# Kernel tuning notes

Measured on AMD Instinct MI355X. Metric: run time of the kernel, lower is better.

## Reference

```python
import jax, jax.numpy as jnp
import numpy as np

DIM = 512
HID = 1536          # int(2*(4*512)/3) rounded up to multiple of 256
N_EXPERTS = 8
TOP_K = 2
SHARED_HID = HID * 2  # n_shared_experts scales hidden dim of the single shared MLP
B, S = 4, 2048


def _swiglu(x, w1, w3, w2):
    return (jax.nn.silu(x @ w1.T) * (x @ w3.T)) @ w2.T


def setup_inputs() -> dict:
    key = jax.random.key(0)
    ks = jax.random.split(key, 8)
    sc_d = 1.0 / np.sqrt(DIM)
    sc_h = 1.0 / np.sqrt(HID)
    sc_sh = 1.0 / np.sqrt(SHARED_HID)
    return {
        "x": jax.random.normal(ks[0], (B, S, DIM), jnp.float32),
        "gate_w": jax.random.normal(ks[1], (N_EXPERTS, DIM), jnp.float32) * sc_d,
        "w1": jax.random.normal(ks[2], (N_EXPERTS, HID, DIM), jnp.float32) * sc_d,
        "w3": jax.random.normal(ks[3], (N_EXPERTS, HID, DIM), jnp.float32) * sc_d,
        "w2": jax.random.normal(ks[4], (N_EXPERTS, DIM, HID), jnp.float32) * sc_h,
        "sw1": jax.random.normal(ks[5], (SHARED_HID, DIM), jnp.float32) * sc_d,
        "sw3": jax.random.normal(ks[6], (SHARED_HID, DIM), jnp.float32) * sc_d,
        "sw2": jax.random.normal(ks[7], (DIM, SHARED_HID), jnp.float32) * sc_sh,
    }


def reference(x, gate_w, w1, w3, w2, sw1, sw3, sw2):
    b, s, d = x.shape
    t = b * s
    xf = x.reshape(t, d)

    # --- gate (greedy top-k over softmax scores, fp32) ---
    logits = xf.astype(jnp.float32) @ gate_w.astype(jnp.float32).T  # [T, E]
    scores = jax.nn.softmax(logits, axis=-1)
    topk_w, topk_i = jax.lax.top_k(scores, TOP_K)                    # [T, K]

    # per-token combine weight for each expert: sum of topk weights routed to it
    e = gate_w.shape[0]
    comb = jnp.zeros((t, e), jnp.float32).at[jnp.arange(t)[:, None], topk_i].add(topk_w)

    # --- routed experts: weighted sum of SwiGLU outputs ---
    y = jnp.zeros((t, d), x.dtype)
    for i in range(e):  # fixed small number of structurally distinct experts
        ye = _swiglu(xf, w1[i], w3[i], w2[i]).astype(x.dtype)
        y = y + comb[:, i:i + 1].astype(x.dtype) * ye
    y = y.reshape(b, s, d)

    # --- shared expert added to all tokens ---
    shared = _swiglu(xf, sw1, sw3, sw2).reshape(b, s, d).astype(x.dtype)
    return y + shared
```

## Files before the change

kernel.cpp:

```cpp
#include <hip/hip_runtime.h>

#define T_TOK 8192
#define DIMSZ 512
#define HIDSZ 1536
#define SHIDSZ 3072
#define NE 8

typedef __attribute__((ext_vector_type(4))) float f32x4;
typedef __attribute__((ext_vector_type(8))) short s16x8;

__device__ __forceinline__ unsigned short f2bf(float f) {
  unsigned int u = __float_as_uint(f);
  u += 0x7fff + ((u >> 16) & 1);
  return (unsigned short)(u >> 16);
}

__device__ __forceinline__ void async16(void* lds, const void* g) {
  __builtin_amdgcn_global_load_lds((const __attribute__((address_space(1))) void*)g,
                                   (__attribute__((address_space(3))) void*)lds,
                                   16, 0, 0);
}

__global__ void cvt_bf16(const float* __restrict__ s, unsigned short* __restrict__ d, int n4) {
  int i = blockIdx.x * blockDim.x + threadIdx.x;
  if (i < n4) {
    float4 v = ((const float4*)s)[i];
    ushort4 o;
    o.x = f2bf(v.x); o.y = f2bf(v.y); o.z = f2bf(v.z); o.w = f2bf(v.w);
    ((ushort4*)d)[i] = o;
  }
}

#define GATE_BLOCKS 256
#define GATE_TPB (T_TOK / GATE_BLOCKS)
#define GATE_TPW (GATE_TPB / 4)

__global__ __launch_bounds__(256) void gate_kernel(
    const float* __restrict__ x, const float* __restrict__ gw,
    float* __restrict__ tw, int* __restrict__ ti, int* __restrict__ cnt) {
  __shared__ int lcnt[NE];
  const int tid = threadIdx.x;
  if (tid < NE) lcnt[tid] = 0;
  __syncthreads();
  const int w = tid >> 6, l = tid & 63;

  float gv[NE][8];
  const float* gbase = gw + l * 8;
#pragma unroll
  for (int e = 0; e < NE; ++e)
#pragma unroll
    for (int j = 0; j < 8; ++j) gv[e][j] = gbase[e * DIMSZ + j];

  const int tok0 = blockIdx.x * GATE_TPB + w * GATE_TPW;
  for (int it = 0; it < GATE_TPW; ++it) {
    const int t = tok0 + it;
    const float* xr = x + (size_t)t * DIMSZ + l * 8;
    float xv[8];
#pragma unroll
    for (int j = 0; j < 8; ++j) xv[j] = xr[j];
    float p[NE];
#pragma unroll
    for (int e = 0; e < NE; ++e) {
      float s = 0.f;
#pragma unroll
      for (int j = 0; j < 8; ++j) s = fmaf(xv[j], gv[e][j], s);
      p[e] = s;
    }
#pragma unroll
    for (int e = 0; e < NE; ++e) {
      float v = p[e];
#pragma unroll
      for (int off = 32; off > 0; off >>= 1) v += __shfl_xor(v, off);
      p[e] = v;
    }
    float m = p[0];
#pragma unroll
    for (int e = 1; e < NE; ++e) m = fmaxf(m, p[e]);
    float ex[NE], s = 0.f;
#pragma unroll
    for (int e = 0; e < NE; ++e) { ex[e] = __expf(p[e] - m); s += ex[e]; }
    float inv = 1.f / s;
    int e0 = 0; float v0 = p[0];
#pragma unroll
    for (int e = 1; e < NE; ++e) if (p[e] > v0) { v0 = p[e]; e0 = e; }
    int e1 = -1; float v1 = -3.4e38f;
#pragma unroll
    for (int e = 0; e < NE; ++e) if (e != e0 && p[e] > v1) { v1 = p[e]; e1 = e; }
    if (l == 0) {
      ti[2 * t] = e0;     tw[2 * t] = ex[e0] * inv;
      ti[2 * t + 1] = e1; tw[2 * t + 1] = ex[e1] * inv;
      atomicAdd(&lcnt[e0], 1);
      atomicAdd(&lcnt[e1], 1);
    }
  }
  __syncthreads();
  if (tid < NE) atomicAdd(&cnt[tid], lcnt[tid]);
}

__global__ void scan_kernel(const int* __restrict__ cnt, int* __restrict__ base,
                            int* __restrict__ cursor) {
  if (threadIdx.x == 0 && blockIdx.x == 0) {
    int r = 0;
    for (int e = 0; e < NE; ++e) { base[e] = r; cursor[e] = r; r += cnt[e]; }
  }
}

__global__ __launch_bounds__(256) void scatter_kernel(
    const int* __restrict__ ti, int* __restrict__ cursor,
    int* __restrict__ tok, int* __restrict__ dst) {
  __shared__ int lcnt[NE], gbase[NE];
  const int tid = threadIdx.x;
  if (tid < NE) lcnt[tid] = 0;
  __syncthreads();
  const int t = blockIdx.x * 256 + tid;
  const int e0 = ti[2 * t], e1 = ti[2 * t + 1];
  const int p0 = atomicAdd(&lcnt[e0], 1);
  const int p1 = atomicAdd(&lcnt[e1], 1);
  __syncthreads();
  if (tid < NE) gbase[tid] = atomicAdd(&cursor[tid], lcnt[tid]);
  __syncthreads();
  const int i0 = gbase[e0] + p0, i1 = gbase[e1] + p1;
  tok[i0] = t; dst[i0] = 2 * t;
  tok[i1] = t; dst[i1] = 2 * t + 1;
}

__global__ void gather_kernel(const unsigned short* __restrict__ xb,
                              const int* __restrict__ tok,
                              unsigned short* __restrict__ xg) {
  int i = blockIdx.x * blockDim.x + threadIdx.x;
  int entry = i >> 6, l = i & 63;
  int t = tok[entry];
  ((uint4*)xg)[entry * 64 + l] = ((const uint4*)xb)[t * 64 + l];
}


template <bool ROUTED>
__global__ __launch_bounds__(256, 3) void gemm1_kernel(
    const unsigned short* __restrict__ A0, const unsigned short* __restrict__ W1,
    const unsigned short* __restrict__ W3, unsigned short* __restrict__ G,
    const int* __restrict__ cnt, const int* __restrict__ base,
    int K, int N, int mtPerE) {
  int e, mt, cntE, rowbase;
  if constexpr (ROUTED) {
    e = blockIdx.x / mtPerE; mt = blockIdx.x % mtPerE;
    cntE = cnt[e];
    if (mt * 128 >= cntE) return;
    rowbase = base[e];
  } else {
    e = 0; mt = blockIdx.x; cntE = T_TOK; rowbase = 0;
  }
  const int m0 = mt * 128;
  const int n0 = blockIdx.y * 64;
  const unsigned short* A = A0 + (size_t)rowbase * K;
  const unsigned short* B1 = W1 + (size_t)e * N * K + (size_t)n0 * K;
  const unsigned short* B3 = W3 + (size_t)e * N * K + (size_t)n0 * K;

  __shared__ __align__(16) unsigned short As[128 * 64];
  __shared__ __align__(16) unsigned short B1s[64 * 64];
  __shared__ __align__(16) unsigned short B3s[64 * 64];

  const int tid = threadIdx.x;
  const int w = tid >> 6, lane = tid & 63;
  const int wr = w >> 1, wc = w & 1;
  const int lhi = lane >> 4, llo = lane & 15;

  const unsigned short* aSrc[4];
  unsigned short* aDst[4];
#pragma unroll
  for (int i = 0; i < 4; ++i) {
    int L = i * 256 + tid, row = L >> 3, c = L & 7, sc = c ^ (row & 7);
    int ar = ROUTED ? min(m0 + row, cntE - 1) : (m0 + row);
    aSrc[i] = A + (size_t)ar * K + sc * 8;
    aDst[i] = &As[(size_t)(i * 256 + (tid & ~63)) * 8];
  }
  const unsigned short *b1Src[2], *b3Src[2];
  unsigned short *b1Dst[2], *b3Dst[2];
#pragma unroll
  for (int i = 0; i < 2; ++i) {
    int L = i * 256 + tid, row = L >> 3, c = L & 7, sc = c ^ (row & 7);
    b1Src[i] = B1 + (size_t)row * K + sc * 8;
    b3Src[i] = B3 + (size_t)row * K + sc * 8;
    b1Dst[i] = &B1s[(size_t)(i * 256 + (tid & ~63)) * 8];
    b3Dst[i] = &B3s[(size_t)(i * 256 + (tid & ~63)) * 8];
  }

  int aOff[4][2], bOff[2][2];
#pragma unroll
  for (int m = 0; m < 4; ++m) {
    int r = wr * 64 + m * 16 + llo;
#pragma unroll
    for (int s = 0; s < 2; ++s)
      aOff[m][s] = r * 64 + (((lhi + 4 * s) ^ (r & 7)) * 8);
  }
#pragma unroll
  for (int n = 0; n < 2; ++n) {
    int r = wc * 32 + n * 16 + llo;
#pragma unroll
    for (int s = 0; s < 2; ++s)
      bOff[n][s] = r * 64 + (((lhi + 4 * s) ^ (r & 7)) * 8);
  }

  f32x4 acc1[4][2], acc3[4][2];
#pragma unroll
  for (int m = 0; m < 4; ++m)
#pragma unroll
    for (int n = 0; n < 2; ++n) {
      acc1[m][n] = f32x4{0.f, 0.f, 0.f, 0.f};
      acc3[m][n] = f32x4{0.f, 0.f, 0.f, 0.f};
    }

  for (int k0 = 0; k0 < K; k0 += 64) {
#pragma unroll
    for (int i = 0; i < 4; ++i) async16(aDst[i], aSrc[i] + k0);
#pragma unroll
    for (int i = 0; i < 2; ++i) {
      async16(b1Dst[i], b1Src[i] + k0);
      async16(b3Dst[i], b3Src[i] + k0);
    }
    __syncthreads();
#pragma unroll
    for (int s = 0; s < 2; ++s) {
      s16x8 a[4], b1f[2], b3f[2];
#pragma unroll
      for (int m = 0; m < 4; ++m) a[m] = *(const s16x8*)&As[aOff[m][s]];
#pragma unroll
      for (int n = 0; n < 2; ++n) {
        b1f[n] = *(const s16x8*)&B1s[bOff[n][s]];
        b3f[n] = *(const s16x8*)&B3s[bOff[n][s]];
      }
#pragma unroll
      for (int m = 0; m < 4; ++m)
#pragma unroll
        for (int n = 0; n < 2; ++n) {
          acc1[m][n] = __builtin_amdgcn_mfma_f32_16x16x32_bf16(a[m], b1f[n], acc1[m][n], 0, 0, 0);
          acc3[m][n] = __builtin_amdgcn_mfma_f32_16x16x32_bf16(a[m], b3f[n], acc3[m][n], 0, 0, 0);
        }
    }
    __syncthreads();
  }

  unsigned short* Grow = G + (size_t)rowbase * N;
#pragma unroll
  for (int m = 0; m < 4; ++m)
#pragma unroll
    for (int n = 0; n < 2; ++n)
#pragma unroll
      for (int q = 0; q < 4; ++q) {
        int r = wr * 64 + m * 16 + lhi * 4 + q;
        if (!ROUTED || (m0 + r) < cntE) {
          float h1 = acc1[m][n][q], h3 = acc3[m][n][q];
          float val = (h1 / (1.f + __expf(-h1))) * h3;
          Grow[(size_t)(m0 + r) * N + n0 + wc * 32 + n * 16 + llo] = f2bf(val);
        }
      }
}

template <bool ROUTED>
__global__ __launch_bounds__(256, 3) void gemm2_kernel(
    const unsigned short* __restrict__ A0, const unsigned short* __restrict__ W2,
    float* __restrict__ Out, const int* __restrict__ cnt, const int* __restrict__ base,
    const int* __restrict__ dst, int K, int mtPerE) {
  int e, mt, cntE, rowbase;
  if constexpr (ROUTED) {
    e = blockIdx.x / mtPerE; mt = blockIdx.x % mtPerE;
    cntE = cnt[e];
    if (mt * 128 >= cntE) return;
    rowbase = base[e];
  } else {
    e = 0; mt = blockIdx.x; cntE = T_TOK; rowbase = 0;
  }
  const int m0 = mt * 128;
  const int n0 = blockIdx.y * 128;
  const unsigned short* A = A0 + (size_t)rowbase * K;
  const unsigned short* B = W2 + (size_t)e * DIMSZ * K + (size_t)n0 * K;

  __shared__ __align__(16) unsigned short As[128 * 64];
  __shared__ __align__(16) unsigned short Bs[128 * 64];

  const int tid = threadIdx.x;
  const int w = tid >> 6, lane = tid & 63;
  const int wr = w >> 1, wc = w & 1;
  const int lhi = lane >> 4, llo = lane & 15;

  const unsigned short *aSrc[4], *bSrc[4];
  unsigned short *aDst[4], *bDst[4];
#pragma unroll
  for (int i = 0; i < 4; ++i) {
    int L = i * 256 + tid, row = L >> 3, c = L & 7, sc = c ^ (row & 7);
    int ar = ROUTED ? min(m0 + row, cntE - 1) : (m0 + row);
    aSrc[i] = A + (size_t)ar * K + sc * 8;
    bSrc[i] = B + (size_t)row * K + sc * 8;
    aDst[i] = &As[(size_t)(i * 256 + (tid & ~63)) * 8];
    bDst[i] = &Bs[(size_t)(i * 256 + (tid & ~63)) * 8];
  }

  int aOff[4][2], bOff[4][2];
#pragma unroll
  for (int m = 0; m < 4; ++m) {
    int ra = wr * 64 + m * 16 + llo;
    int rb = wc * 64 + m * 16 + llo;
#pragma unroll
    for (int s = 0; s < 2; ++s) {
      aOff[m][s] = ra * 64 + (((lhi + 4 * s) ^ (ra & 7)) * 8);
      bOff[m][s] = rb * 64 + (((lhi + 4 * s) ^ (rb & 7)) * 8);
    }
  }

  f32x4 acc[4][4];
#pragma unroll
  for (int i = 0; i < 4; ++i)
#pragma unroll
    for (int j = 0; j < 4; ++j) acc[i][j] = f32x4{0.f, 0.f, 0.f, 0.f};

  for (int k0 = 0; k0 < K; k0 += 64) {
#pragma unroll
    for (int i = 0; i < 4; ++i) {
      async16(aDst[i], aSrc[i] + k0);
      async16(bDst[i], bSrc[i] + k0);
    }
    __syncthreads();
#pragma unroll
    for (int s = 0; s < 2; ++s) {
      s16x8 a[4], b[4];
#pragma unroll
      for (int m = 0; m < 4; ++m) {
        a[m] = *(const s16x8*)&As[aOff[m][s]];
        b[m] = *(const s16x8*)&Bs[bOff[m][s]];
      }
#pragma unroll
      for (int i = 0; i < 4; ++i)
#pragma unroll
        for (int j = 0; j < 4; ++j)
          acc[i][j] = __builtin_amdgcn_mfma_f32_16x16x32_bf16(a[i], b[j], acc[i][j], 0, 0, 0);
    }
    __syncthreads();
  }

#pragma unroll
  for (int i = 0; i < 4; ++i)
#pragma unroll
    for (int j = 0; j < 4; ++j)
#pragma unroll
      for (int q = 0; q < 4; ++q) {
        int r = wr * 64 + i * 16 + lhi * 4 + q;
        if (!ROUTED || (m0 + r) < cntE) {
          int orow;
          if constexpr (ROUTED) orow = dst[rowbase + m0 + r];
          else                  orow = m0 + r;
          Out[(size_t)orow * DIMSZ + n0 + wc * 64 + j * 16 + llo] = acc[i][j][q];
        }
      }
}

__global__ void combine_kernel(const float* __restrict__ shbuf, const float* __restrict__ pair,
                               const float* __restrict__ tw, float* __restrict__ out) {
  int i = blockIdx.x * blockDim.x + threadIdx.x;
  int t = i >> 7, c = i & 127;
  float w0 = tw[2 * t], w1 = tw[2 * t + 1];
  float4 a = ((const float4*)shbuf)[i];
  float4 p0 = ((const float4*)pair)[(size_t)(2 * t) * 128 + c];
  float4 p1 = ((const float4*)pair)[(size_t)(2 * t + 1) * 128 + c];
  float4 o;
  o.x = a.x + w0 * p0.x + w1 * p1.x;
  o.y = a.y + w0 * p0.y + w1 * p1.y;
  o.z = a.z + w0 * p0.z + w1 * p1.z;
  o.w = a.w + w0 * p0.w + w1 * p1.w;
  ((float4*)out)[i] = o;
}

extern "C" void kernel_launch(void* const* d_in, const int* in_sizes, int n_in,
                              void* d_out, int out_size, void* d_ws, size_t ws_size,
                              hipStream_t stream) {
  const float* x   = (const float*)d_in[0];
  const float* gw  = (const float*)d_in[1];
  const float* w1  = (const float*)d_in[2];
  const float* w3  = (const float*)d_in[3];
  const float* w2  = (const float*)d_in[4];
  const float* sw1 = (const float*)d_in[5];
  const float* sw3 = (const float*)d_in[6];
  const float* sw2 = (const float*)d_in[7];
  float* out = (float*)d_out;

  char* p = (char*)d_ws;
  auto alloc = [&](size_t bytes) {
    char* r = p;
    p += (bytes + 255) & ~(size_t)255;
    return r;
  };
  unsigned short* xb   = (unsigned short*)alloc((size_t)T_TOK * DIMSZ * 2);
  unsigned short* xg   = (unsigned short*)alloc((size_t)2 * T_TOK * DIMSZ * 2);
  unsigned short* w1b  = (unsigned short*)alloc((size_t)NE * HIDSZ * DIMSZ * 2);
  unsigned short* w3b  = (unsigned short*)alloc((size_t)NE * HIDSZ * DIMSZ * 2);
  unsigned short* w2b  = (unsigned short*)alloc((size_t)NE * DIMSZ * HIDSZ * 2);
  unsigned short* sw1b = (unsigned short*)alloc((size_t)SHIDSZ * DIMSZ * 2);
  unsigned short* sw3b = (unsigned short*)alloc((size_t)SHIDSZ * DIMSZ * 2);
  unsigned short* sw2b = (unsigned short*)alloc((size_t)DIMSZ * SHIDSZ * 2);
  unsigned short* g    = (unsigned short*)alloc((size_t)T_TOK * SHIDSZ * 2);
  float* pairout = (float*)alloc((size_t)2 * T_TOK * DIMSZ * 4);
  float* shbuf   = (float*)alloc((size_t)T_TOK * DIMSZ * 4);
  float* tw = (float*)alloc((size_t)2 * T_TOK * 4);
  int* ti   = (int*)alloc((size_t)2 * T_TOK * 4);
  int* tok  = (int*)alloc((size_t)2 * T_TOK * 4);
  int* dst  = (int*)alloc((size_t)2 * T_TOK * 4);
  int* meta = (int*)alloc(256);
  int* cnt = meta, *cursor = meta + 8, *base = meta + 16;

  auto cvt = [&](const float* s, unsigned short* d, size_t n) {
    int n4 = (int)(n / 4);
    cvt_bf16<<<(n4 + 255) / 256, 256, 0, stream>>>(s, d, n4);
  };
  cvt(x, xb, (size_t)T_TOK * DIMSZ);
  cvt(w1, w1b, (size_t)NE * HIDSZ * DIMSZ);
  cvt(w3, w3b, (size_t)NE * HIDSZ * DIMSZ);
  cvt(w2, w2b, (size_t)NE * DIMSZ * HIDSZ);
  cvt(sw1, sw1b, (size_t)SHIDSZ * DIMSZ);
  cvt(sw3, sw3b, (size_t)SHIDSZ * DIMSZ);
  cvt(sw2, sw2b, (size_t)DIMSZ * SHIDSZ);

  hipMemsetAsync(meta, 0, 64, stream);
  gate_kernel<<<GATE_BLOCKS, 256, 0, stream>>>(x, gw, tw, ti, cnt);
  scan_kernel<<<1, 64, 0, stream>>>(cnt, base, cursor);
  scatter_kernel<<<T_TOK / 256, 256, 0, stream>>>(ti, cursor, tok, dst);
  gather_kernel<<<(2 * T_TOK * 64) / 256, 256, 0, stream>>>(xb, tok, xg);

  gemm1_kernel<false><<<dim3(T_TOK / 128, SHIDSZ / 64), 256, 0, stream>>>(
      xb, sw1b, sw3b, g, nullptr, nullptr, DIMSZ, SHIDSZ, T_TOK / 128);
  gemm2_kernel<false><<<dim3(T_TOK / 128, DIMSZ / 128), 256, 0, stream>>>(
      g, sw2b, shbuf, nullptr, nullptr, nullptr, SHIDSZ, T_TOK / 128);

  gemm1_kernel<true><<<dim3(NE * (T_TOK / 128), HIDSZ / 64), 256, 0, stream>>>(
      xg, w1b, w3b, g, cnt, base, DIMSZ, HIDSZ, T_TOK / 128);
  gemm2_kernel<true><<<dim3(NE * (T_TOK / 128), DIMSZ / 128), 256, 0, stream>>>(
      g, w2b, pairout, cnt, base, dst, HIDSZ, T_TOK / 128);

  combine_kernel<<<(T_TOK * 128) / 256, 256, 0, stream>>>(shbuf, pairout, tw, out);
}
```

Measured before the change: 448.7 us.

## Double-buffer LDS in both GEMMs and halve gemm2 M-tile

Both GEMM kernels now use two LDS buffers. The next K-tile is prefetched with async global-to-LDS loads while the current tile is computed, and partial vmcnt waits plus raw barriers replace the full __syncthreads pairs, so memory latency overlaps with MFMA work. gemm2 also drops from a 128-row to a 64-row M tile, which doubles its grid for better CU fill and cuts padding waste on the routed experts. The cost is doubled LDS use, which lowers gemm1's occupancy hint from 3 to 2 blocks, and less B-tile reuse in gemm2.

```diff
diff --git a/kernel.cpp b/kernel.cpp
--- a/kernel.cpp
+++ b/kernel.cpp
@@ -8,6 +8,8 @@
 
 typedef __attribute__((ext_vector_type(4))) float f32x4;
 typedef __attribute__((ext_vector_type(8))) short s16x8;
+
+#define SBAR() __builtin_amdgcn_s_barrier()
 
 __device__ __forceinline__ unsigned short f2bf(float f) {
   unsigned int u = __float_as_uint(f);
@@ -135,7 +137,7 @@
 
 
 template <bool ROUTED>
-__global__ __launch_bounds__(256, 3) void gemm1_kernel(
+__global__ __launch_bounds__(256, 2) void gemm1_kernel(
     const unsigned short* __restrict__ A0, const unsigned short* __restrict__ W1,
     const unsigned short* __restrict__ W3, unsigned short* __restrict__ G,
     const int* __restrict__ cnt, const int* __restrict__ base,
@@ -155,9 +157,9 @@
   const unsigned short* B1 = W1 + (size_t)e * N * K + (size_t)n0 * K;
   const unsigned short* B3 = W3 + (size_t)e * N * K + (size_t)n0 * K;
 
-  __shared__ __align__(16) unsigned short As[128 * 64];
-  __shared__ __align__(16) unsigned short B1s[64 * 64];
-  __shared__ __align__(16) unsigned short B3s[64 * 64];
+  __shared__ __align__(16) unsigned short As[2 * 128 * 64];
+  __shared__ __align__(16) unsigned short B1s[2 * 64 * 64];
+  __shared__ __align__(16) unsigned short B3s[2 * 64 * 64];
 
   const int tid = threadIdx.x;
   const int w = tid >> 6, lane = tid & 63;
@@ -165,23 +167,22 @@
   const int lhi = lane >> 4, llo = lane & 15;
 
   const unsigned short* aSrc[4];
-  unsigned short* aDst[4];
+  int aDst[4];
 #pragma unroll
   for (int i = 0; i < 4; ++i) {
     int L = i * 256 + tid, row = L >> 3, c = L & 7, sc = c ^ (row & 7);
     int ar = ROUTED ? min(m0 + row, cntE - 1) : (m0 + row);
     aSrc[i] = A + (size_t)ar * K + sc * 8;
-    aDst[i] = &As[(size_t)(i * 256 + (tid & ~63)) * 8];
+    aDst[i] = (i * 256 + (tid & ~63)) * 8;
   }
   const unsigned short *b1Src[2], *b3Src[2];
-  unsigned short *b1Dst[2], *b3Dst[2];
+  int bDst[2];
 #pragma unroll
   for (int i = 0; i < 2; ++i) {
     int L = i * 256 + tid, row = L >> 3, c = L & 7, sc = c ^ (row & 7);
     b1Src[i] = B1 + (size_t)row * K + sc * 8;
     b3Src[i] = B3 + (size_t)row * K + sc * 8;
-    b1Dst[i] = &B1s[(size_t)(i * 256 + (tid & ~63)) * 8];
-    b3Dst[i] = &B3s[(size_t)(i * 256 + (tid & ~63)) * 8];
+    bDst[i] = (i * 256 + (tid & ~63)) * 8;
   }
 
   int aOff[4][2], bOff[2][2];
@@ -209,24 +210,43 @@
       acc3[m][n] = f32x4{0.f, 0.f, 0.f, 0.f};
     }
 
-  for (int k0 = 0; k0 < K; k0 += 64) {
-#pragma unroll
-    for (int i = 0; i < 4; ++i) async16(aDst[i], aSrc[i] + k0);
-#pragma unroll
-    for (int i = 0; i < 2; ++i) {
-      async16(b1Dst[i], b1Src[i] + k0);
-      async16(b3Dst[i], b3Src[i] + k0);
-    }
-    __syncthreads();
+  const int nt = K >> 6;
+  int cur = 0;
+#pragma unroll
+  for (int i = 0; i < 4; ++i) async16(&As[aDst[i]], aSrc[i]);
+#pragma unroll
+  for (int i = 0; i < 2; ++i) {
+    async16(&B1s[bDst[i]], b1Src[i]);
+    async16(&B3s[bDst[i]], b3Src[i]);
+  }
+
+  for (int t = 0; t < nt; ++t) {
+    const bool more = (t + 1) < nt;
+    if (more) {
+      const int k1 = (t + 1) << 6;
+      const int nxtA = (cur ^ 1) * 8192, nxtB = (cur ^ 1) * 4096;
+#pragma unroll
+      for (int i = 0; i < 4; ++i) async16(&As[nxtA + aDst[i]], aSrc[i] + k1);
+#pragma unroll
+      for (int i = 0; i < 2; ++i) {
+        async16(&B1s[nxtB + bDst[i]], b1Src[i] + k1);
+        async16(&B3s[nxtB + bDst[i]], b3Src[i] + k1);
+      }
+      asm volatile("s_waitcnt vmcnt(8)" ::: "memory");
+    } else {
+      asm volatile("s_waitcnt vmcnt(0)" ::: "memory");
+    }
+    SBAR();
+    const int cA = cur * 8192, cB = cur * 4096;
 #pragma unroll
     for (int s = 0; s < 2; ++s) {
       s16x8 a[4], b1f[2], b3f[2];
 #pragma unroll
-      for (int m = 0; m < 4; ++m) a[m] = *(const s16x8*)&As[aOff[m][s]];
+      for (int m = 0; m < 4; ++m) a[m] = *(const s16x8*)&As[cA + aOff[m][s]];
 #pragma unroll
       for (int n = 0; n < 2; ++n) {
-        b1f[n] = *(const s16x8*)&B1s[bOff[n][s]];
-        b3f[n] = *(const s16x8*)&B3s[bOff[n][s]];
+        b1f[n] = *(const s16x8*)&B1s[cB + bOff[n][s]];
+        b3f[n] = *(const s16x8*)&B3s[cB + bOff[n][s]];
       }
 #pragma unroll
       for (int m = 0; m < 4; ++m)
@@ -236,7 +256,7 @@
           acc3[m][n] = __builtin_amdgcn_mfma_f32_16x16x32_bf16(a[m], b3f[n], acc3[m][n], 0, 0, 0);
         }
     }
-    __syncthreads();
+    if (more) { SBAR(); cur ^= 1; }
   }
 
   unsigned short* Grow = G + (size_t)rowbase * N;
@@ -264,85 +284,109 @@
   if constexpr (ROUTED) {
     e = blockIdx.x / mtPerE; mt = blockIdx.x % mtPerE;
     cntE = cnt[e];
-    if (mt * 128 >= cntE) return;
+    if (mt * 64 >= cntE) return;
     rowbase = base[e];
   } else {
     e = 0; mt = blockIdx.x; cntE = T_TOK; rowbase = 0;
   }
-  const int m0 = mt * 128;
+  const int m0 = mt * 64;
   const int n0 = blockIdx.y * 128;
   const unsigned short* A = A0 + (size_t)rowbase * K;
   const unsigned short* B = W2 + (size_t)e * DIMSZ * K + (size_t)n0 * K;
 
-  __shared__ __align__(16) unsigned short As[128 * 64];
-  __shared__ __align__(16) unsigned short Bs[128 * 64];
+  __shared__ __align__(16) unsigned short As[2 * 64 * 64];
+  __shared__ __align__(16) unsigned short Bs[2 * 128 * 64];
 
   const int tid = threadIdx.x;
   const int w = tid >> 6, lane = tid & 63;
   const int wr = w >> 1, wc = w & 1;
   const int lhi = lane >> 4, llo = lane & 15;
 
-  const unsigned short *aSrc[4], *bSrc[4];
-  unsigned short *aDst[4], *bDst[4];
-#pragma unroll
-  for (int i = 0; i < 4; ++i) {
+  const unsigned short* aSrc[2];
+  int aDst[2];
+#pragma unroll
+  for (int i = 0; i < 2; ++i) {
     int L = i * 256 + tid, row = L >> 3, c = L & 7, sc = c ^ (row & 7);
     int ar = ROUTED ? min(m0 + row, cntE - 1) : (m0 + row);
     aSrc[i] = A + (size_t)ar * K + sc * 8;
+    aDst[i] = (i * 256 + (tid & ~63)) * 8;
+  }
+  const unsigned short* bSrc[4];
+  int bDst[4];
+#pragma unroll
+  for (int i = 0; i < 4; ++i) {
+    int L = i * 256 + tid, row = L >> 3, c = L & 7, sc = c ^ (row & 7);
     bSrc[i] = B + (size_t)row * K + sc * 8;
-    aDst[i] = &As[(size_t)(i * 256 + (tid & ~63)) * 8];
-    bDst[i] = &Bs[(size_t)(i * 256 + (tid & ~63)) * 8];
-  }
-
-  int aOff[4][2], bOff[4][2];
-#pragma unroll
-  for (int m = 0; m < 4; ++m) {
-    int ra = wr * 64 + m * 16 + llo;
-    int rb = wc * 64 + m * 16 + llo;
+    bDst[i] = (i * 256 + (tid & ~63)) * 8;
+  }
+
+  int aOff[2][2], bOff[4][2];
+#pragma unroll
+  for (int m = 0; m < 2; ++m) {
+    int r = wr * 32 + m * 16 + llo;
+#pragma unroll
+    for (int s = 0; s < 2; ++s)
+      aOff[m][s] = r * 64 + (((lhi + 4 * s) ^ (r & 7)) * 8);
+  }
+#pragma unroll
+  for (int n = 0; n < 4; ++n) {
+    int r = wc * 64 + n * 16 + llo;
+#pragma unroll
+    for (int s = 0; s < 2; ++s)
+      bOff[n][s] = r * 64 + (((lhi + 4 * s) ^ (r & 7)) * 8);
+  }
+
+  f32x4 acc[2][4];
+#pragma unroll
+  for (int i = 0; i < 2; ++i)
+#pragma unroll
+    for (int j = 0; j < 4; ++j) acc[i][j] = f32x4{0.f, 0.f, 0.f, 0.f};
+
+  const int nt = K >> 6;
+  int cur = 0;
+#pragma unroll
+  for (int i = 0; i < 2; ++i) async16(&As[aDst[i]], aSrc[i]);
+#pragma unroll
+  for (int i = 0; i < 4; ++i) async16(&Bs[bDst[i]], bSrc[i]);
+
+  for (int t = 0; t < nt; ++t) {
+    const bool more = (t + 1) < nt;
+    if (more) {
+      const int k1 = (t + 1) << 6;
+      const int nxtA = (cur ^ 1) * 4096, nxtB = (cur ^ 1) * 8192;
+#pragma unroll
+      for (int i = 0; i < 2; ++i) async16(&As[nxtA + aDst[i]], aSrc[i] + k1);
+#pragma unroll
+      for (int i = 0; i < 4; ++i) async16(&Bs[nxtB + bDst[i]], bSrc[i] + k1);
+      asm volatile("s_waitcnt vmcnt(6)" ::: "memory");
+    } else {
+      asm volatile("s_waitcnt vmcnt(0)" ::: "memory");
+    }
+    SBAR();
+    const int cA = cur * 4096, cB = cur * 8192;
 #pragma unroll
     for (int s = 0; s < 2; ++s) {
-      aOff[m][s] = ra * 64 + (((lhi + 4 * s) ^ (ra & 7)) * 8);
-      bOff[m][s] = rb * 64 + (((lhi + 4 * s) ^ (rb & 7)) * 8);
-    }
-  }
-
-  f32x4 acc[4][4];
-#pragma unroll
-  for (int i = 0; i < 4; ++i)
-#pragma unroll
-    for (int j = 0; j < 4; ++j) acc[i][j] = f32x4{0.f, 0.f, 0.f, 0.f};
-
-  for (int k0 = 0; k0 < K; k0 += 64) {
-#pragma unroll
-    for (int i = 0; i < 4; ++i) {
-      async16(aDst[i], aSrc[i] + k0);
-      async16(bDst[i], bSrc[i] + k0);
-    }
-    __syncthreads();
-#pragma unroll
-    for (int s = 0; s < 2; ++s) {
-      s16x8 a[4], b[4];
-#pragma unroll
-      for (int m = 0; m < 4; ++m) {
-        a[m] = *(const s16x8*)&As[aOff[m][s]];
-        b[m] = *(const s16x8*)&Bs[bOff[m][s]];
-      }
-#pragma unroll
-      for (int i = 0; i < 4; ++i)
+      s16x8 a[2], b[4];
+#pragma unroll
+      for (int m = 0; m < 2; ++m) a[m] = *(const s16x8*)&As[cA + aOff[m][s]];
+#pragma unroll
+      for (int n = 0; n < 4; ++n) b[n] = *(const s16x8*)&Bs[cB + bOff[n][s]];
+#pragma unroll
+      for (int i = 0; i < 2; ++i)
 #pragma unroll
         for (int j = 0; j < 4; ++j)
           acc[i][j] = __builtin_amdgcn_mfma_f32_16x16x32_bf16(a[i], b[j], acc[i][j], 0, 0, 0);
     }
-    __syncthreads();
-  }
-
-#pragma unroll
-  for (int i = 0; i < 4; ++i)
+    if (more) { SBAR(); cur ^= 1; }
+  }
+
+#pragma unroll
+  for (int i = 0; i < 2; ++i)
 #pragma unroll
     for (int j = 0; j < 4; ++j)
 #pragma unroll
       for (int q = 0; q < 4; ++q) {
-        int r = wr * 64 + i * 16 + lhi * 4 + q;
+        int r = wr * 32 + i * 16 + lhi * 4 + q;
         if (!ROUTED || (m0 + r) < cntE) {
           int orow;
           if constexpr (ROUTED) orow = dst[rowbase + m0 + r];
@@ -425,13 +469,13 @@
 
   gemm1_kernel<false><<<dim3(T_TOK / 128, SHIDSZ / 64), 256, 0, stream>>>(
       xb, sw1b, sw3b, g, nullptr, nullptr, DIMSZ, SHIDSZ, T_TOK / 128);
-  gemm2_kernel<false><<<dim3(T_TOK / 128, DIMSZ / 128), 256, 0, stream>>>(
-      g, sw2b, shbuf, nullptr, nullptr, nullptr, SHIDSZ, T_TOK / 128);
+  gemm2_kernel<false><<<dim3(T_TOK / 64, DIMSZ / 128), 256, 0, stream>>>(
+      g, sw2b, shbuf, nullptr, nullptr, nullptr, SHIDSZ, T_TOK / 64);
 
   gemm1_kernel<true><<<dim3(NE * (T_TOK / 128), HIDSZ / 64), 256, 0, stream>>>(
       xg, w1b, w3b, g, cnt, base, DIMSZ, HIDSZ, T_TOK / 128);
-  gemm2_kernel<true><<<dim3(NE * (T_TOK / 128), DIMSZ / 128), 256, 0, stream>>>(
-      g, w2b, pairout, cnt, base, dst, HIDSZ, T_TOK / 128);
+  gemm2_kernel<true><<<dim3(NE * (T_TOK / 64), DIMSZ / 128), 256, 0, stream>>>(
+      g, w2b, pairout, cnt, base, dst, HIDSZ, T_TOK / 64);
 
   combine_kernel<<<(T_TOK * 128) / 256, 256, 0, stream>>>(shbuf, pairout, tw, out);
 }
```

Result: slower. 500.7 us (+11.6%).
